# Kernel optimization log

Measured on AMD Instinct MI355X. Metric: run time of the kernel, lower is better.

The kernel has to match this reference:

```python
import jax, jax.numpy as jnp
import numpy as np

N = 40000      # nodes
E = 640000     # edges (avg degree 16)
D = 128        # feature dim (in_features == all hidden_dims due to residual)


def setup_inputs() -> dict:
    key = jax.random.key(0)
    ks = jax.random.split(key, 8)
    xavier = (6.0 / (D + D)) ** 0.5
    return {
        "x": jax.random.normal(ks[0], (N, D), dtype=jnp.float32),
        "edge_index": jax.random.randint(ks[1], (2, E), 0, N, dtype=jnp.int64),
        "W_t": jax.random.uniform(ks[2], (D, D), jnp.float32, -xavier, xavier),
        "b_t": jnp.zeros((D,), jnp.float32),
        "W0": jax.random.uniform(ks[3], (D, D), jnp.float32, -xavier, xavier),
        "b0": jnp.zeros((D,), jnp.float32),
        "W1": jax.random.uniform(ks[4], (D, D), jnp.float32, -xavier, xavier),
        "b1": jnp.zeros((D,), jnp.float32),
    }


def _gcn_layer(h, row, col, W, b):
    # linear transform, then edge-wise gather + scatter-add aggregation
    z = jnp.matmul(h, W)                                  # [N, D]
    agg = jnp.zeros_like(z).at[row].add(z[col])           # out[row] += z[col]
    return jax.nn.relu(agg + b)


def reference(x, edge_index, W_t, b_t, W0, b0, W1, b1):
    row, col = edge_index[0], edge_index[1]
    h = jnp.matmul(x, W_t) + b_t                          # self.transform
    # residual GCN layers (dropout p=0.0 -> identity; eval mode)
    h = h + _gcn_layer(h, row, col, W0, b0)
    h = h + _gcn_layer(h, row, col, W1, b1)
    return h
```

## Files before the change

### kernel.cpp

```cpp
#include <hip/hip_runtime.h>
#include <hip/hip_bf16.h>

#define N_NODES 40000
#define N_EDGES 640000
#define DIM     128
#define NB      157
#define GEMMB   625
#define HEB     1250
#define CHUNKS  64
#define CHUNK_E 10000
#define LDSW    10000

typedef __attribute__((ext_vector_type(8))) short short8;
typedef __attribute__((ext_vector_type(4))) float f32x4;
typedef __attribute__((ext_vector_type(2))) float f32x2;

__device__ inline short f2bf(float f) {
    __hip_bfloat16 h = __float2bfloat16(f);
    return *reinterpret_cast<short*>(&h);
}
__device__ inline float bf2f(short u) {
    union { unsigned int i; float f; } x;
    x.i = ((unsigned int)(unsigned short)u) << 16;
    return x.f;
}

__device__ inline int fragidx(int k, int n) {
    int kb = k >> 5, kq = (k >> 3) & 3, j = k & 7;
    int nt = n >> 4, nl = n & 15;
    return (((kb * 8 + nt) * 64 + kq * 16 + nl) * 8 + j);
}

__global__ __launch_bounds__(256) void prep_zero(const float* __restrict__ Wt,
                                                 const float* __restrict__ W0,
                                                 const float* __restrict__ W1,
                                                 const float* __restrict__ bt,
                                                 short* __restrict__ WtF,
                                                 short* __restrict__ WfF,
                                                 short* __restrict__ W1F,
                                                 float* __restrict__ btf,
                                                 int* __restrict__ flagtot) {
    int b = blockIdx.x;
    if (b < 64) {
        int gid = b * 256 + threadIdx.x;
        int k = gid >> 7, n = gid & 127;
        float wf = 0.f;
        for (int kk = 0; kk < 128; ++kk)
            wf += Wt[k * 128 + kk] * W0[kk * 128 + n];
        int fi = fragidx(k, n);
        WtF[fi] = f2bf(Wt[k * 128 + n]);
        W1F[fi] = f2bf(W1[k * 128 + n]);
        WfF[fi] = f2bf(wf);
        if (gid < 128) {
            float s = 0.f;
            for (int kk = 0; kk < 128; ++kk) s += bt[kk] * W0[kk * 128 + n];
            btf[n] = s;
        }
    } else {
        flagtot[threadIdx.x]       = 0;
        flagtot[threadIdx.x + 256] = 0;
    }
}

__global__ __launch_bounds__(256) void histlds_gemm(const int* __restrict__ rows,
                                                    unsigned char* __restrict__ rank8,
                                                    unsigned int* __restrict__ cnt8w,
                                                    const float* __restrict__ A,
                                                    const short* __restrict__ WtF,
                                                    const short* __restrict__ WfF,
                                                    const float* __restrict__ bt,
                                                    const float* __restrict__ btf,
                                                    float* __restrict__ H,
                                                    __hip_bfloat16* __restrict__ Z) {
    __shared__ unsigned int lcnt[LDSW];

    if (blockIdx.x < CHUNKS) {
        for (int i = threadIdx.x; i < LDSW; i += 256) lcnt[i] = 0u;
        __syncthreads();
        const int base = blockIdx.x * CHUNK_E;
#pragma unroll
        for (int i = 0; i < 40; ++i) {
            int o = i * 256 + threadIdx.x;
            if (o < CHUNK_E) {
                int e = base + o;
                int r = rows[e];
                unsigned int sh = (unsigned int)(r & 3) * 8u;
                unsigned int old = atomicAdd(&lcnt[r >> 2], 1u << sh);
                rank8[e] = (unsigned char)((old >> sh) & 0xFFu);
            }
        }
        __syncthreads();
        unsigned int* out = cnt8w + blockIdx.x * LDSW;
        for (int i = threadIdx.x; i < LDSW; i += 256) out[i] = lcnt[i];
        return;
    }

    const int t    = threadIdx.x;
    const int wave = t >> 6;
    const int l    = t & 63;
    const int nl   = l & 15;
    const int quad = l >> 4;
    const int wRow = (blockIdx.x - CHUNKS) * 64 + wave * 16;

    f32x4 accH[8], accZ[8];
#pragma unroll
    for (int nt = 0; nt < 8; ++nt) {
        accH[nt] = (f32x4){0.f, 0.f, 0.f, 0.f};
        accZ[nt] = (f32x4){0.f, 0.f, 0.f, 0.f};
    }

#pragma unroll
    for (int kb = 0; kb < 4; ++kb) {
        const float* ap = A + (size_t)(wRow + nl) * 128 + kb * 32 + quad * 8;
        float4 f0 = *(const float4*)ap;
        float4 f1 = *(const float4*)(ap + 4);
        short8 afrag;
        afrag[0] = f2bf(f0.x); afrag[1] = f2bf(f0.y);
        afrag[2] = f2bf(f0.z); afrag[3] = f2bf(f0.w);
        afrag[4] = f2bf(f1.x); afrag[5] = f2bf(f1.y);
        afrag[6] = f2bf(f1.z); afrag[7] = f2bf(f1.w);
#pragma unroll
        for (int nt = 0; nt < 8; ++nt) {
            int off = ((kb * 8 + nt) * 64 + l) * 8;
            short8 bt_frag = *(const short8*)&WtF[off];
            short8 bf_frag = *(const short8*)&WfF[off];
            accH[nt] = __builtin_amdgcn_mfma_f32_16x16x32_bf16(afrag, bt_frag, accH[nt], 0, 0, 0);
            accZ[nt] = __builtin_amdgcn_mfma_f32_16x16x32_bf16(afrag, bf_frag, accZ[nt], 0, 0, 0);
        }
    }

#pragma unroll
    for (int nt = 0; nt < 8; ++nt) {
        int col = nt * 16 + nl;
        float bH = bt[col];
        float bZ = btf[col];
#pragma unroll
        for (int r = 0; r < 4; ++r) {
            int row = wRow + quad * 4 + r;
            H[(size_t)row * 128 + col] = accH[nt][r] + bH;
            *(short*)&Z[(size_t)row * 128 + col] = f2bf(accZ[nt][r] + bZ);
        }
    }
}

__global__ __launch_bounds__(256) void scan_onepass(unsigned char* __restrict__ cnt8,
                                                    int* __restrict__ flags,
                                                    int* __restrict__ totals,
                                                    int* __restrict__ row_ptr) {
    __shared__ int sh[256];
    const int b = blockIdx.x;
    const int t = threadIdx.x;
    const int i = b * 256 + t;

    int deg = 0;
    if (i < N_NODES) {
#pragma unroll 8
        for (int c = 0; c < CHUNKS; ++c) deg += cnt8[(size_t)c * N_NODES + i];
    }

    int val = deg;
    sh[t] = val;
    __syncthreads();
    for (int off = 1; off < 256; off <<= 1) {
        int a = (t >= off) ? sh[t - off] : 0;
        __syncthreads();
        val += a;
        sh[t] = val;
        __syncthreads();
    }
    const int excl  = val - deg;
    const int total = sh[255];

    if (t == 0) {
        atomicExch(&totals[b], total);
        __threadfence();
        atomicExch(&flags[b], 1);
    }

    int v = 0;
    if (t < NB) {
        while (atomicAdd(&flags[t], 0) == 0) { }
        v = atomicAdd(&totals[t], 0);
    }
    __syncthreads();
    int val2 = v;
    sh[t] = val2;
    __syncthreads();
    for (int off = 1; off < 256; off <<= 1) {
        int a = (t >= off) ? sh[t - off] : 0;
        __syncthreads();
        val2 += a;
        sh[t] = val2;
        __syncthreads();
    }
    int blkOff = (b == 0) ? 0 : sh[b - 1];

    if (i < N_NODES) {
        int base = excl + blkOff;
        row_ptr[i] = base;
        int run = 0;
#pragma unroll 8
        for (int c = 0; c < CHUNKS; ++c) {
            int cv = cnt8[(size_t)c * N_NODES + i];
            cnt8[(size_t)c * N_NODES + i] = (unsigned char)run;
            run += cv;
        }
    }
    if (i == 0) row_ptr[N_NODES] = N_EDGES;
}

__global__ __launch_bounds__(256) void scatter_plain(const int* __restrict__ rows,
                                                     const int* __restrict__ cols,
                                                     const unsigned char* __restrict__ rank8,
                                                     const unsigned char* __restrict__ pref8,
                                                     const int* __restrict__ row_ptr,
                                                     unsigned short* __restrict__ adj) {
    int gid = blockIdx.x * 256 + threadIdx.x;
#pragma unroll
    for (int h = 0; h < 2; ++h) {
        int e = gid + h * HEB * 256;
        int r = rows[e];
        int c = e / CHUNK_E;
        int pos = row_ptr[r] + (int)pref8[(size_t)c * N_NODES + r] + (int)rank8[e];
        adj[pos] = (unsigned short)cols[e];
    }
}

__global__ __launch_bounds__(256) void agg0_gemm(const __hip_bfloat16* __restrict__ z0,
                                                 const int* __restrict__ row_ptr,
                                                 const unsigned short* __restrict__ adj,
                                                 const float* __restrict__ bias,
                                                 const short* __restrict__ W1F,
                                                 float* __restrict__ H,
                                                 unsigned char* __restrict__ Z1) {
    __shared__ short hs[16][136];

    const int t    = threadIdx.x;
    const int wave = t >> 6;
    const int l    = t & 63;
    const int quad = l >> 4;
    const int sl   = l & 15;
    const int nodeBase = blockIdx.x * 16;

#pragma unroll
    for (int u = 0; u < 4; ++u) {
        const int m    = wave * 4 + u;
        const int node = nodeBase + m;
        const int s = row_ptr[node];
        const int e = row_ptr[node + 1];

        float acc[8];
#pragma unroll
        for (int j = 0; j < 8; ++j) acc[j] = 0.f;

        int it = s + quad;
        for (; it + 12 < e; it += 16) {
            int c0 = adj[it];
            int c1 = adj[it + 4];
            int c2 = adj[it + 8];
            int c3 = adj[it + 12];
            short8 v0 = *(const short8*)&z0[(size_t)c0 * DIM + sl * 8];
            short8 v1 = *(const short8*)&z0[(size_t)c1 * DIM + sl * 8];
            short8 v2 = *(const short8*)&z0[(size_t)c2 * DIM + sl * 8];
            short8 v3 = *(const short8*)&z0[(size_t)c3 * DIM + sl * 8];
#pragma unroll
            for (int j = 0; j < 8; ++j)
                acc[j] += (bf2f(v0[j]) + bf2f(v1[j])) + (bf2f(v2[j]) + bf2f(v3[j]));
        }
        for (; it + 4 < e; it += 8) {
            int c0 = adj[it];
            int c1 = adj[it + 4];
            short8 v0 = *(const short8*)&z0[(size_t)c0 * DIM + sl * 8];
            short8 v1 = *(const short8*)&z0[(size_t)c1 * DIM + sl * 8];
#pragma unroll
            for (int j = 0; j < 8; ++j) acc[j] += bf2f(v0[j]) + bf2f(v1[j]);
        }
        if (it < e) {
            int c = adj[it];
            short8 v = *(const short8*)&z0[(size_t)c * DIM + sl * 8];
#pragma unroll
            for (int j = 0; j < 8; ++j) acc[j] += bf2f(v[j]);
        }

#pragma unroll
        for (int j = 0; j < 8; ++j) acc[j] += __shfl_xor(acc[j], 16, 64);
#pragma unroll
        for (int j = 0; j < 8; ++j) acc[j] += __shfl_xor(acc[j], 32, 64);

        if (quad == 0) {
            float* hp = H + (size_t)node * DIM + sl * 8;
            float4 h0 = *(float4*)hp;
            float4 h1 = *(float4*)(hp + 4);
            float4 b0v = *(const float4*)&bias[sl * 8];
            float4 b1v = *(const float4*)&bias[sl * 8 + 4];
            float r[8];
            r[0] = acc[0] + b0v.x; r[1] = acc[1] + b0v.y; r[2] = acc[2] + b0v.z; r[3] = acc[3] + b0v.w;
            r[4] = acc[4] + b1v.x; r[5] = acc[5] + b1v.y; r[6] = acc[6] + b1v.z; r[7] = acc[7] + b1v.w;
            float hn[8];
            hn[0] = h0.x; hn[1] = h0.y; hn[2] = h0.z; hn[3] = h0.w;
            hn[4] = h1.x; hn[5] = h1.y; hn[6] = h1.z; hn[7] = h1.w;
            short8 o;
#pragma unroll
            for (int j = 0; j < 8; ++j) {
                float rr = r[j] > 0.f ? r[j] : 0.f;
                hn[j] += rr;
                o[j] = f2bf(hn[j]);
            }
            *(float4*)hp       = make_float4(hn[0], hn[1], hn[2], hn[3]);
            *(float4*)(hp + 4) = make_float4(hn[4], hn[5], hn[6], hn[7]);
            *(short8*)&hs[m][sl * 8] = o;
        }
    }
    __syncthreads();

    f32x4 acc2[2];
    acc2[0] = (f32x4){0.f, 0.f, 0.f, 0.f};
    acc2[1] = (f32x4){0.f, 0.f, 0.f, 0.f};
#pragma unroll
    for (int kb = 0; kb < 4; ++kb) {
        short8 afrag = *(const short8*)&hs[sl][kb * 32 + quad * 8];
#pragma unroll
        for (int nt2 = 0; nt2 < 2; ++nt2) {
            int nt = wave * 2 + nt2;
            short8 bfrag = *(const short8*)&W1F[((kb * 8 + nt) * 64 + l) * 8];
            acc2[nt2] = __builtin_amdgcn_mfma_f32_16x16x32_bf16(afrag, bfrag, acc2[nt2], 0, 0, 0);
        }
    }
#pragma unroll
    for (int nt2 = 0; nt2 < 2; ++nt2) {
        int col = (wave * 2 + nt2) * 16 + sl;
#pragma unroll
        for (int r = 0; r < 4; ++r) {
            int row = nodeBase + quad * 4 + r;
            float v = acc2[nt2][r];
            int packed = __builtin_amdgcn_cvt_pk_fp8_f32(v, v, 0, false);
            Z1[(size_t)row * 128 + col] = (unsigned char)(packed & 0xFF);
        }
    }
}

__global__ __launch_bounds__(256) void agg_final(const unsigned char* __restrict__ z1,
                                                 const int* __restrict__ row_ptr,
                                                 const unsigned short* __restrict__ adj,
                                                 const float* __restrict__ bias,
                                                 float* __restrict__ H) {
    const int wave = threadIdx.x >> 6;
    const int l    = threadIdx.x & 63;
    const int quad = l >> 4;
    const int sl   = l & 15;
    const int node = blockIdx.x * 4 + wave;
    if (node >= N_NODES) return;

    const int s = row_ptr[node];
    const int e = row_ptr[node + 1];

    float acc[8];
#pragma unroll
    for (int j = 0; j < 8; ++j) acc[j] = 0.f;

#define ADD_FP8(u2)                                                          \
    {                                                                        \
        f32x2 a0 = __builtin_amdgcn_cvt_pk_f32_fp8((u2).x, false);           \
        f32x2 a1 = __builtin_amdgcn_cvt_pk_f32_fp8((u2).x, true);            \
        f32x2 a2 = __builtin_amdgcn_cvt_pk_f32_fp8((u2).y, false);           \
        f32x2 a3 = __builtin_amdgcn_cvt_pk_f32_fp8((u2).y, true);            \
        acc[0] += a0.x; acc[1] += a0.y; acc[2] += a1.x; acc[3] += a1.y;      \
        acc[4] += a2.x; acc[5] += a2.y; acc[6] += a3.x; acc[7] += a3.y;      \
    }

    int it = s + quad;
    for (; it + 12 < e; it += 16) {
        int c0 = adj[it];
        int c1 = adj[it + 4];
        int c2 = adj[it + 8];
        int c3 = adj[it + 12];
        uint2 v0 = *(const uint2*)&z1[(size_t)c0 * 128 + sl * 8];
        uint2 v1 = *(const uint2*)&z1[(size_t)c1 * 128 + sl * 8];
        uint2 v2 = *(const uint2*)&z1[(size_t)c2 * 128 + sl * 8];
        uint2 v3 = *(const uint2*)&z1[(size_t)c3 * 128 + sl * 8];
        ADD_FP8(v0); ADD_FP8(v1); ADD_FP8(v2); ADD_FP8(v3);
    }
    for (; it + 4 < e; it += 8) {
        int c0 = adj[it];
        int c1 = adj[it + 4];
        uint2 v0 = *(const uint2*)&z1[(size_t)c0 * 128 + sl * 8];
        uint2 v1 = *(const uint2*)&z1[(size_t)c1 * 128 + sl * 8];
        ADD_FP8(v0); ADD_FP8(v1);
    }
    if (it < e) {
        int c = adj[it];
        uint2 v = *(const uint2*)&z1[(size_t)c * 128 + sl * 8];
        ADD_FP8(v);
    }
#undef ADD_FP8

#pragma unroll
    for (int j = 0; j < 8; ++j) acc[j] += __shfl_xor(acc[j], 16, 64);
#pragma unroll
    for (int j = 0; j < 8; ++j) acc[j] += __shfl_xor(acc[j], 32, 64);

    if (quad == 0) {
        float* hp = H + (size_t)node * DIM + sl * 8;
        float4 h0 = *(float4*)hp;
        float4 h1 = *(float4*)(hp + 4);
        float4 b0 = *(const float4*)&bias[sl * 8];
        float4 b1 = *(const float4*)&bias[sl * 8 + 4];
        float r0 = acc[0] + b0.x, r1 = acc[1] + b0.y, r2 = acc[2] + b0.z, r3 = acc[3] + b0.w;
        float r4 = acc[4] + b1.x, r5 = acc[5] + b1.y, r6 = acc[6] + b1.z, r7 = acc[7] + b1.w;
        h0.x += r0 > 0.f ? r0 : 0.f;  h0.y += r1 > 0.f ? r1 : 0.f;
        h0.z += r2 > 0.f ? r2 : 0.f;  h0.w += r3 > 0.f ? r3 : 0.f;
        h1.x += r4 > 0.f ? r4 : 0.f;  h1.y += r5 > 0.f ? r5 : 0.f;
        h1.z += r6 > 0.f ? r6 : 0.f;  h1.w += r7 > 0.f ? r7 : 0.f;
        *(float4*)hp       = h0;
        *(float4*)(hp + 4) = h1;
    }
}

extern "C" void kernel_launch(void* const* d_in, const int* in_sizes, int n_in,
                              void* d_out, int out_size, void* d_ws, size_t ws_size,
                              hipStream_t stream) {
    const float* x   = (const float*)d_in[0];
    const int*   ei  = (const int*)d_in[1];
    const float* W_t = (const float*)d_in[2];
    const float* b_t = (const float*)d_in[3];
    const float* W0  = (const float*)d_in[4];
    const float* b0  = (const float*)d_in[5];
    const float* W1  = (const float*)d_in[6];
    const float* b1  = (const float*)d_in[7];

    const int* rows = ei;
    const int* cols = ei + N_EDGES;

    float* H = (float*)d_out;

    char* w = (char*)d_ws;
    __hip_bfloat16* Z0 = (__hip_bfloat16*)w;  w += (size_t)N_NODES * DIM * 2;
    unsigned char*  Z1 = (unsigned char*)w;   w += (size_t)N_NODES * DIM;
    short* WtF = (short*)w;  w += 128 * 128 * 2;
    short* WfF = (short*)w;  w += 128 * 128 * 2;
    short* W1F = (short*)w;  w += 128 * 128 * 2;
    float* btf = (float*)w;  w += 128 * 4;
    int* row_ptr = (int*)w;  w += (N_NODES + 1) * 4;
    int* flags   = (int*)w;  w += 256 * 4;
    int* totals  = (int*)w;  w += 256 * 4;
    unsigned int* cnt8w = (unsigned int*)w;  w += (size_t)CHUNKS * LDSW * 4;
    unsigned char* rank8 = (unsigned char*)w;  w += (size_t)N_EDGES;
    unsigned short* adj  = (unsigned short*)w;

    const int aggBlocks = (N_NODES + 3) / 4;

    prep_zero<<<65, 256, 0, stream>>>(W_t, W0, W1, b_t, WtF, WfF, W1F, btf, flags);

    histlds_gemm<<<CHUNKS + GEMMB, 256, 0, stream>>>(rows, rank8, cnt8w,
                                                     x, WtF, WfF, b_t, btf, H, Z0);

    scan_onepass<<<NB, 256, 0, stream>>>((unsigned char*)cnt8w, flags, totals, row_ptr);

    scatter_plain<<<HEB, 256, 0, stream>>>(rows, cols, rank8, (unsigned char*)cnt8w,
                                           row_ptr, adj);

    agg0_gemm<<<N_NODES / 16, 256, 0, stream>>>(Z0, row_ptr, adj, b0, W1F, H, Z1);

    agg_final<<<aggBlocks, 256, 0, stream>>>(Z1, row_ptr, adj, b1, H);
}
```

Baseline: 185.2 us.

## Fuse prep, histogram, scan, scatter and GEMM into one kernel with spin-wait dependencies

Replaces four separate launches (weight prep, histogram+GEMM, decoupled scan, edge scatter) with a single mega kernel. Block ranges take on each role and wait on global atomic counters for their predecessors, so the dense GEMM can overlap with the graph preprocessing and inter-kernel gaps go away. Per-chunk degree counts are packed as 4-bit nibbles, which halves LDS and the count buffer but assumes no node gets more than 15 edges within a chunk. Prefix offsets move to a separate buffer, and the sync area is cleared with a memset. The spin waits depend on blocks being dispatched in order and enough of them being resident at once, or the kernel can deadlock.

```diff
diff --git a/kernel.cpp b/kernel.cpp
--- a/kernel.cpp
+++ b/kernel.cpp
@@ -6,10 +6,17 @@
 #define DIM     128
 #define NB      157
 #define GEMMB   625
-#define HEB     1250
+#define SCATB   313
 #define CHUNKS  64
 #define CHUNK_E 10000
-#define LDSW    10000
+#define LDSW    5000
+
+#define B_PREP  0
+#define B_HIST  64
+#define B_SCAN  128
+#define B_SCAT  285
+#define B_GEMM  598
+#define B_TOT   1223
 
 typedef __attribute__((ext_vector_type(8))) short short8;
 typedef __attribute__((ext_vector_type(4))) float f32x4;
@@ -31,18 +38,37 @@
     return (((kb * 8 + nt) * 64 + kq * 16 + nl) * 8 + j);
 }
 
-__global__ __launch_bounds__(256) void prep_zero(const float* __restrict__ Wt,
-                                                 const float* __restrict__ W0,
-                                                 const float* __restrict__ W1,
-                                                 const float* __restrict__ bt,
-                                                 short* __restrict__ WtF,
-                                                 short* __restrict__ WfF,
-                                                 short* __restrict__ W1F,
-                                                 float* __restrict__ btf,
-                                                 int* __restrict__ flagtot) {
-    int b = blockIdx.x;
-    if (b < 64) {
-        int gid = b * 256 + threadIdx.x;
+__global__ __launch_bounds__(256, 6) void mega(const int* __restrict__ rows,
+                                               const int* __restrict__ cols,
+                                               const float* __restrict__ Wt,
+                                               const float* __restrict__ W0,
+                                               const float* __restrict__ W1,
+                                               const float* __restrict__ bt,
+                                               short* __restrict__ WtF,
+                                               short* __restrict__ WfF,
+                                               short* __restrict__ W1F,
+                                               float* __restrict__ btf,
+                                               int* __restrict__ syncbuf,
+                                               unsigned int* __restrict__ cnt4w,
+                                               unsigned char* __restrict__ rank8,
+                                               unsigned char* __restrict__ pref8,
+                                               int* __restrict__ row_ptr,
+                                               unsigned short* __restrict__ adj,
+                                               const float* __restrict__ A,
+                                               float* __restrict__ H,
+                                               __hip_bfloat16* __restrict__ Z) {
+    __shared__ unsigned int lcnt[LDSW];
+    int* prepDone = syncbuf + 0;
+    int* histDone = syncbuf + 1;
+    int* scanDone = syncbuf + 2;
+    int* flags    = syncbuf + 3;
+    int* totals   = syncbuf + 3 + 256;
+
+    const int b = blockIdx.x;
+    const int t = threadIdx.x;
+
+    if (b < B_HIST) {
+        int gid = b * 256 + t;
         int k = gid >> 7, n = gid & 127;
         float wf = 0.f;
         for (int kk = 0; kk < 128; ++kk)
@@ -56,51 +82,140 @@
             for (int kk = 0; kk < 128; ++kk) s += bt[kk] * W0[kk * 128 + n];
             btf[n] = s;
         }
-    } else {
-        flagtot[threadIdx.x]       = 0;
-        flagtot[threadIdx.x + 256] = 0;
-    }
-}
-
-__global__ __launch_bounds__(256) void histlds_gemm(const int* __restrict__ rows,
-                                                    unsigned char* __restrict__ rank8,
-                                                    unsigned int* __restrict__ cnt8w,
-                                                    const float* __restrict__ A,
-                                                    const short* __restrict__ WtF,
-                                                    const short* __restrict__ WfF,
-                                                    const float* __restrict__ bt,
-                                                    const float* __restrict__ btf,
-                                                    float* __restrict__ H,
-                                                    __hip_bfloat16* __restrict__ Z) {
-    __shared__ unsigned int lcnt[LDSW];
-
-    if (blockIdx.x < CHUNKS) {
-        for (int i = threadIdx.x; i < LDSW; i += 256) lcnt[i] = 0u;
-        __syncthreads();
-        const int base = blockIdx.x * CHUNK_E;
+        __syncthreads();
+        if (t == 0) { __threadfence(); atomicAdd(prepDone, 1); }
+        return;
+    }
+
+    if (b < B_SCAN) {
+        const int c = b - B_HIST;
+        for (int i = t; i < LDSW; i += 256) lcnt[i] = 0u;
+        __syncthreads();
+        const int base = c * CHUNK_E;
 #pragma unroll
         for (int i = 0; i < 40; ++i) {
-            int o = i * 256 + threadIdx.x;
+            int o = i * 256 + t;
             if (o < CHUNK_E) {
                 int e = base + o;
                 int r = rows[e];
-                unsigned int sh = (unsigned int)(r & 3) * 8u;
-                unsigned int old = atomicAdd(&lcnt[r >> 2], 1u << sh);
-                rank8[e] = (unsigned char)((old >> sh) & 0xFFu);
+                unsigned int sh4 = (unsigned int)(r & 7) * 4u;
+                unsigned int old = atomicAdd(&lcnt[r >> 3], 1u << sh4);
+                rank8[e] = (unsigned char)((old >> sh4) & 0xFu);
             }
         }
         __syncthreads();
-        unsigned int* out = cnt8w + blockIdx.x * LDSW;
-        for (int i = threadIdx.x; i < LDSW; i += 256) out[i] = lcnt[i];
+        unsigned int* out = cnt4w + c * LDSW;
+        for (int i = t; i < LDSW; i += 256) out[i] = lcnt[i];
+        __syncthreads();
+        if (t == 0) { __threadfence(); atomicAdd(histDone, 1); }
         return;
     }
 
-    const int t    = threadIdx.x;
+    if (b < B_SCAT) {
+        const int sb = b - B_SCAN;
+        int* sh = (int*)lcnt;
+        if (t == 0) {
+            while (atomicAdd(histDone, 0) < CHUNKS) __builtin_amdgcn_s_sleep(2);
+            __threadfence();
+        }
+        __syncthreads();
+
+        const int i = sb * 256 + t;
+        int deg = 0;
+        if (i < N_NODES) {
+            int wi = i >> 3;
+            unsigned int sh4 = (unsigned int)(i & 7) * 4u;
+#pragma unroll 8
+            for (int c = 0; c < CHUNKS; ++c)
+                deg += (int)((cnt4w[c * LDSW + wi] >> sh4) & 0xFu);
+        }
+
+        int val = deg;
+        sh[t] = val;
+        __syncthreads();
+        for (int off = 1; off < 256; off <<= 1) {
+            int a = (t >= off) ? sh[t - off] : 0;
+            __syncthreads();
+            val += a;
+            sh[t] = val;
+            __syncthreads();
+        }
+        const int excl  = val - deg;
+        const int total = sh[255];
+
+        if (t == 0) {
+            atomicExch(&totals[sb], total);
+            __threadfence();
+            atomicExch(&flags[sb], 1);
+        }
+        int v = 0;
+        if (t < NB) {
+            while (atomicAdd(&flags[t], 0) == 0) __builtin_amdgcn_s_sleep(2);
+            v = atomicAdd(&totals[t], 0);
+        }
+        __syncthreads();
+        int val2 = v;
+        sh[t] = val2;
+        __syncthreads();
+        for (int off = 1; off < 256; off <<= 1) {
+            int a = (t >= off) ? sh[t - off] : 0;
+            __syncthreads();
+            val2 += a;
+            sh[t] = val2;
+            __syncthreads();
+        }
+        int blkOff = (sb == 0) ? 0 : sh[sb - 1];
+
+        if (i < N_NODES) {
+            row_ptr[i] = excl + blkOff;
+            int wi = i >> 3;
+            unsigned int sh4 = (unsigned int)(i & 7) * 4u;
+            int run = 0;
+#pragma unroll 8
+            for (int c = 0; c < CHUNKS; ++c) {
+                int cv = (int)((cnt4w[c * LDSW + wi] >> sh4) & 0xFu);
+                pref8[(size_t)c * N_NODES + i] = (unsigned char)run;
+                run += cv;
+            }
+        }
+        if (i == 0) row_ptr[N_NODES] = N_EDGES;
+        __syncthreads();
+        if (t == 0) { __threadfence(); atomicAdd(scanDone, 1); }
+        return;
+    }
+
+    if (b < B_GEMM) {
+        const int cb = b - B_SCAT;
+        if (t == 0) {
+            while (atomicAdd(scanDone, 0) < NB) __builtin_amdgcn_s_sleep(2);
+            __threadfence();
+        }
+        __syncthreads();
+        int gid = cb * 256 + t;
+#pragma unroll
+        for (int h = 0; h < 8; ++h) {
+            int e = gid + h * SCATB * 256;
+            if (e < N_EDGES) {
+                int r = rows[e];
+                int c = e / CHUNK_E;
+                int pos = row_ptr[r] + (int)pref8[(size_t)c * N_NODES + r] + (int)rank8[e];
+                adj[pos] = (unsigned short)cols[e];
+            }
+        }
+        return;
+    }
+
+    if (t == 0) {
+        while (atomicAdd(prepDone, 0) < 64) __builtin_amdgcn_s_sleep(2);
+        __threadfence();
+    }
+    __syncthreads();
+
     const int wave = t >> 6;
     const int l    = t & 63;
     const int nl   = l & 15;
     const int quad = l >> 4;
-    const int wRow = (blockIdx.x - CHUNKS) * 64 + wave * 16;
+    const int wRow = (b - B_GEMM) * 64 + wave * 16;
 
     f32x4 accH[8], accZ[8];
 #pragma unroll
@@ -140,89 +255,6 @@
             H[(size_t)row * 128 + col] = accH[nt][r] + bH;
             *(short*)&Z[(size_t)row * 128 + col] = f2bf(accZ[nt][r] + bZ);
         }
-    }
-}
-
-__global__ __launch_bounds__(256) void scan_onepass(unsigned char* __restrict__ cnt8,
-                                                    int* __restrict__ flags,
-                                                    int* __restrict__ totals,
-                                                    int* __restrict__ row_ptr) {
-    __shared__ int sh[256];
-    const int b = blockIdx.x;
-    const int t = threadIdx.x;
-    const int i = b * 256 + t;
-
-    int deg = 0;
-    if (i < N_NODES) {
-#pragma unroll 8
-        for (int c = 0; c < CHUNKS; ++c) deg += cnt8[(size_t)c * N_NODES + i];
-    }
-
-    int val = deg;
-    sh[t] = val;
-    __syncthreads();
-    for (int off = 1; off < 256; off <<= 1) {
-        int a = (t >= off) ? sh[t - off] : 0;
-        __syncthreads();
-        val += a;
-        sh[t] = val;
-        __syncthreads();
-    }
-    const int excl  = val - deg;
-    const int total = sh[255];
-
-    if (t == 0) {
-        atomicExch(&totals[b], total);
-        __threadfence();
-        atomicExch(&flags[b], 1);
-    }
-
-    int v = 0;
-    if (t < NB) {
-        while (atomicAdd(&flags[t], 0) == 0) { }
-        v = atomicAdd(&totals[t], 0);
-    }
-    __syncthreads();
-    int val2 = v;
-    sh[t] = val2;
-    __syncthreads();
-    for (int off = 1; off < 256; off <<= 1) {
-        int a = (t >= off) ? sh[t - off] : 0;
-        __syncthreads();
-        val2 += a;
-        sh[t] = val2;
-        __syncthreads();
-    }
-    int blkOff = (b == 0) ? 0 : sh[b - 1];
-
-    if (i < N_NODES) {
-        int base = excl + blkOff;
-        row_ptr[i] = base;
-        int run = 0;
-#pragma unroll 8
-        for (int c = 0; c < CHUNKS; ++c) {
-            int cv = cnt8[(size_t)c * N_NODES + i];
-            cnt8[(size_t)c * N_NODES + i] = (unsigned char)run;
-            run += cv;
-        }
-    }
-    if (i == 0) row_ptr[N_NODES] = N_EDGES;
-}
-
-__global__ __launch_bounds__(256) void scatter_plain(const int* __restrict__ rows,
-                                                     const int* __restrict__ cols,
-                                                     const unsigned char* __restrict__ rank8,
-                                                     const unsigned char* __restrict__ pref8,
-                                                     const int* __restrict__ row_ptr,
-                                                     unsigned short* __restrict__ adj) {
-    int gid = blockIdx.x * 256 + threadIdx.x;
-#pragma unroll
-    for (int h = 0; h < 2; ++h) {
-        int e = gid + h * HEB * 256;
-        int r = rows[e];
-        int c = e / CHUNK_E;
-        int pos = row_ptr[r] + (int)pref8[(size_t)c * N_NODES + r] + (int)rank8[e];
-        adj[pos] = (unsigned short)cols[e];
     }
 }
 
@@ -441,23 +473,20 @@
     short* W1F = (short*)w;  w += 128 * 128 * 2;
     float* btf = (float*)w;  w += 128 * 4;
     int* row_ptr = (int*)w;  w += (N_NODES + 1) * 4;
-    int* flags   = (int*)w;  w += 256 * 4;
-    int* totals  = (int*)w;  w += 256 * 4;
-    unsigned int* cnt8w = (unsigned int*)w;  w += (size_t)CHUNKS * LDSW * 4;
+    int* syncbuf = (int*)w;  w += 520 * 4;
+    unsigned int* cnt4w = (unsigned int*)w;  w += (size_t)CHUNKS * LDSW * 4;
+    unsigned char* pref8 = (unsigned char*)w;  w += (size_t)CHUNKS * N_NODES;
     unsigned char* rank8 = (unsigned char*)w;  w += (size_t)N_EDGES;
     unsigned short* adj  = (unsigned short*)w;
 
     const int aggBlocks = (N_NODES + 3) / 4;
 
-    prep_zero<<<65, 256, 0, stream>>>(W_t, W0, W1, b_t, WtF, WfF, W1F, btf, flags);
-
-    histlds_gemm<<<CHUNKS + GEMMB, 256, 0, stream>>>(rows, rank8, cnt8w,
-                                                     x, WtF, WfF, b_t, btf, H, Z0);
-
-    scan_onepass<<<NB, 256, 0, stream>>>((unsigned char*)cnt8w, flags, totals, row_ptr);
-
-    scatter_plain<<<HEB, 256, 0, stream>>>(rows, cols, rank8, (unsigned char*)cnt8w,
-                                           row_ptr, adj);
+    hipMemsetAsync(syncbuf, 0, 520 * sizeof(int), stream);
+
+    mega<<<B_TOT, 256, 0, stream>>>(rows, cols, W_t, W0, W1, b_t,
+                                    WtF, WfF, W1F, btf, syncbuf,
+                                    cnt4w, rank8, pref8, row_ptr, adj,
+                                    x, H, Z0);
 
     agg0_gemm<<<N_NODES / 16, 256, 0, stream>>>(Z0, row_ptr, adj, b0, W1F, H, Z1);
 
```

New measurement: 262.6 us. 41.8% more time.
